# Performance work log

Measured on AMD Instinct MI355X. Metric: run time of the kernel, lower is better.

## Reference

```python
import jax, jax.numpy as jnp
import numpy as np

B, NUM_OBJ, R, D, C = 1024, 128, 32, 512, 7  # scans, obj slots, rel samples, feat dim, rel classes
N = NUM_OBJ + R  # 160 graph nodes per scan


def setup_inputs() -> dict:
    key = jax.random.key(0)
    ks = jax.random.split(key, 8)
    obj_feats = jax.random.normal(ks[0], (B, NUM_OBJ, D), jnp.float32)
    pairs = jax.random.randint(ks[1], (B, R, 2), 0, NUM_OBJ, dtype=jnp.int32)
    init = lambda k, shape, fan_in: jax.random.normal(k, shape, jnp.float32) / np.float32(np.sqrt(fan_in))
    return {
        "obj_feats": obj_feats,
        "pairs": pairs,
        "fuse_w": init(ks[2], (2 * D, D), 2 * D), "fuse_b": jnp.zeros((D,), jnp.float32),
        "gcn_w": init(ks[3], (D, D), D), "gcn_b": jnp.zeros((D,), jnp.float32),
        "fc1_w": init(ks[4], (D, 256), D), "fc1_b": jnp.zeros((256,), jnp.float32),
        "fc2_w": init(ks[5], (256, 128), 256), "fc2_b": jnp.zeros((128,), jnp.float32),
        "fc3_w": init(ks[6], (128, C), 128), "fc3_b": jnp.zeros((C,), jnp.float32),
    }


def reference(obj_feats, pairs, fuse_w, fuse_b, gcn_w, gcn_b,
              fc1_w, fc1_b, fc2_w, fc2_b, fc3_w, fc3_b):
    # --- init_rel_node (pos_fuse=False): fuse sub/obj features per sampled pair ---
    sub = jnp.take_along_axis(obj_feats, pairs[:, :, 0:1], axis=1)  # [B,R,D]
    obj = jnp.take_along_axis(obj_feats, pairs[:, :, 1:2], axis=1)  # [B,R,D]
    init_rel = jnp.concatenate([sub, obj], axis=-1) @ fuse_w + fuse_b  # [B,R,D]

    # --- X: object node feats in rows [0,NUM_OBJ), rel node feats in rows [NUM_OBJ,N) ---
    X = jnp.concatenate([obj_feats, init_rel], axis=1)  # [B,N,D]

    # --- A: get_graph_gcn_with_rel -- scatter 4 directed edges per pair ---
    b_idx = jnp.arange(B)[:, None]                      # [B,1]
    ridx = NUM_OBJ + jnp.arange(R)[None, :]             # [1,R] rel node index j+num_obj
    p0, p1 = pairs[:, :, 0], pairs[:, :, 1]             # [B,R]
    A = jnp.zeros((B, N, N), jnp.float32)
    A = A.at[b_idx, p0, ridx].set(1.0)
    A = A.at[b_idx, ridx, p1].set(1.0)
    A = A.at[b_idx, p1, ridx].set(1.0)
    A = A.at[b_idx, ridx, p0].set(1.0)

    # --- simpleGCN: relu((A @ X) W + b) ---
    H = jax.nn.relu(jnp.einsum('bnm,bmd->bnd', A, X) @ gcn_w + gcn_b)  # [B,N,D]

    # --- residual: GCN rel-node output + init rel feats ---
    rel_feat = H[:, NUM_OBJ:, :] + init_rel  # [B,R,D]

    # --- proxi_detector (dropout = identity, eval behavior) ---
    h = jax.nn.relu(rel_feat @ fc1_w + fc1_b)
    h = jax.nn.relu(h @ fc2_w + fc2_b)
    logits = h @ fc3_w + fc3_b  # [B,R,C]
    return jax.nn.softmax(logits, axis=-1)
```

## Files before the change

### kernel.cpp

```cpp
#include <hip/hip_runtime.h>
#include <hip/hip_bf16.h>

#define B_    1024
#define NOBJ  128
#define RREL  32
#define DIM   512
#define MTOT  32768

typedef __bf16 bf16x8 __attribute__((ext_vector_type(8)));
typedef float  f32x4  __attribute__((ext_vector_type(4)));

__device__ __forceinline__ unsigned short f2bf(float f) {
    unsigned int u = __float_as_uint(f);
    u += 0x7FFFu + ((u >> 16) & 1u);
    return (unsigned short)(u >> 16);
}
__device__ __forceinline__ float bf2f(unsigned short h) {
    return __uint_as_float(((unsigned int)h) << 16);
}

__device__ __forceinline__ void load16_to_lds(const unsigned short* g, unsigned short* l) {
    __builtin_amdgcn_global_load_lds((const __attribute__((address_space(1))) void*)g,
                                     (__attribute__((address_space(3))) void*)l,
                                     16, 0, 0);
}

__global__ __launch_bounds__(256) void gather_kernel(
        const float* __restrict__ obj, const int* __restrict__ pairs,
        unsigned short* __restrict__ As, unsigned short* __restrict__ Msum) {
    int t = threadIdx.x;
    int base = blockIdx.x * 8;
    for (int rr = 0; rr < 8; ++rr) {
        int m  = base + rr;
        int b  = m >> 5;
        int p0 = pairs[(m << 1) + 0];
        int p1 = pairs[(m << 1) + 1];
        const float* srow = obj + (size_t)(b * NOBJ + p0) * DIM;
        const float* orow = obj + (size_t)(b * NOBJ + p1) * DIM;
        float2 s2 = *(const float2*)(srow + 2 * t);
        float2 o2 = *(const float2*)(orow + 2 * t);
        size_t arow = (size_t)m * 1024;
        *(ushort2*)(As + arow + 2 * t)       = make_ushort2(f2bf(s2.x), f2bf(s2.y));
        *(ushort2*)(As + arow + DIM + 2 * t) = make_ushort2(f2bf(o2.x), f2bf(o2.y));
        float mx = s2.x, my = s2.y;
        if (p0 != p1) { mx += o2.x; my += o2.y; }
        *(ushort2*)(Msum + (size_t)m * DIM + 2 * t) = make_ushort2(f2bf(mx), f2bf(my));
    }
}

__global__ __launch_bounds__(256) void transpose_tile(
        const float* __restrict__ in, unsigned short* __restrict__ out,
        int K, int N) {
    __shared__ float t32[32][33];
    int t  = threadIdx.x;
    int tx = t & 31, ty = t >> 5;
    int bk = blockIdx.x * 32, bn = blockIdx.y * 32;
#pragma unroll
    for (int i = 0; i < 4; ++i)
        t32[ty + i * 8][tx] = in[(size_t)(bk + ty + i * 8) * N + bn + tx];
    __syncthreads();
#pragma unroll
    for (int i = 0; i < 4; ++i)
        out[(size_t)(bn + ty + i * 8) * K + bk + tx] = f2bf(t32[tx][ty + i * 8]);
}

__global__ __launch_bounds__(256) void gemm_fused12(
        const unsigned short* __restrict__ As,
        const unsigned short* __restrict__ Msum,
        const unsigned short* __restrict__ WfT,
        const unsigned short* __restrict__ WgT,
        const float* __restrict__ fuse_b, const float* __restrict__ gcn_b,
        unsigned short* __restrict__ rf) {
    __shared__ __align__(16) unsigned short ldsA[128 * 32];
    __shared__ __align__(16) unsigned short ldsB[128 * 32];

    int tid  = threadIdx.x;
    int wid  = tid >> 6;
    int lane = tid & 63;
    int wm   = wid & 1;
    int wn   = wid >> 1;
    int m0   = blockIdx.x * 128;
    int n0   = blockIdx.y * 128;

    f32x4 accF[4][4], accG[4][4];
#pragma unroll
    for (int i = 0; i < 4; ++i)
#pragma unroll
        for (int j = 0; j < 4; ++j)
#pragma unroll
            for (int k = 0; k < 4; ++k) { accF[i][j][k] = 0.0f; accG[i][j][k] = 0.0f; }

    int r = tid >> 2, c = tid & 3;
    unsigned short* la0 = ldsA + wid * 512;
    unsigned short* la1 = ldsA + 2048 + wid * 512;
    unsigned short* lb0 = ldsB + wid * 512;
    unsigned short* lb1 = ldsB + 2048 + wid * 512;

    int arow = wm * 64 + (lane & 15);
    int brow = wn * 64 + (lane & 15);
    int koff = (lane >> 4) * 8;

    {
        const unsigned short* ag0 = As + (size_t)(m0 + r)      * 1024 + c * 8;
        const unsigned short* ag1 = As + (size_t)(m0 + 64 + r) * 1024 + c * 8;
        const unsigned short* bg0 = WfT + (size_t)(n0 + r)      * 1024 + c * 8;
        const unsigned short* bg1 = WfT + (size_t)(n0 + 64 + r) * 1024 + c * 8;
        for (int k0 = 0; k0 < 1024; k0 += 32) {
            __syncthreads();
            load16_to_lds(ag0 + k0, la0);
            load16_to_lds(ag1 + k0, la1);
            load16_to_lds(bg0 + k0, lb0);
            load16_to_lds(bg1 + k0, lb1);
            __syncthreads();
            bf16x8 a[4], b[4];
#pragma unroll
            for (int i = 0; i < 4; ++i)
                a[i] = *(const bf16x8*)(ldsA + (arow + i * 16) * 32 + koff);
#pragma unroll
            for (int j = 0; j < 4; ++j)
                b[j] = *(const bf16x8*)(ldsB + (brow + j * 16) * 32 + koff);
#pragma unroll
            for (int i = 0; i < 4; ++i)
#pragma unroll
                for (int j = 0; j < 4; ++j)
                    accF[i][j] = __builtin_amdgcn_mfma_f32_16x16x32_bf16(a[i], b[j], accF[i][j], 0, 0, 0);
        }
    }
    {
        const unsigned short* ag0 = Msum + (size_t)(m0 + r)      * 512 + c * 8;
        const unsigned short* ag1 = Msum + (size_t)(m0 + 64 + r) * 512 + c * 8;
        const unsigned short* bg0 = WgT + (size_t)(n0 + r)      * 512 + c * 8;
        const unsigned short* bg1 = WgT + (size_t)(n0 + 64 + r) * 512 + c * 8;
        for (int k0 = 0; k0 < 512; k0 += 32) {
            __syncthreads();
            load16_to_lds(ag0 + k0, la0);
            load16_to_lds(ag1 + k0, la1);
            load16_to_lds(bg0 + k0, lb0);
            load16_to_lds(bg1 + k0, lb1);
            __syncthreads();
            bf16x8 a[4], b[4];
#pragma unroll
            for (int i = 0; i < 4; ++i)
                a[i] = *(const bf16x8*)(ldsA + (arow + i * 16) * 32 + koff);
#pragma unroll
            for (int j = 0; j < 4; ++j)
                b[j] = *(const bf16x8*)(ldsB + (brow + j * 16) * 32 + koff);
#pragma unroll
            for (int i = 0; i < 4; ++i)
#pragma unroll
                for (int j = 0; j < 4; ++j)
                    accG[i][j] = __builtin_amdgcn_mfma_f32_16x16x32_bf16(a[i], b[j], accG[i][j], 0, 0, 0);
        }
    }

    int crow  = wm * 64 + (lane >> 4) * 4;
    int ccol0 = wn * 64 + (lane & 15);
    float bf_[4], bg_[4];
#pragma unroll
    for (int j = 0; j < 4; ++j) {
        bf_[j] = fuse_b[n0 + ccol0 + j * 16];
        bg_[j] = gcn_b [n0 + ccol0 + j * 16];
    }
#pragma unroll
    for (int i = 0; i < 4; ++i)
#pragma unroll
        for (int j = 0; j < 4; ++j) {
            int col = n0 + ccol0 + j * 16;
#pragma unroll
            for (int jj = 0; jj < 4; ++jj) {
                int row = m0 + crow + i * 16 + jj;
                float v = fmaxf(accG[i][j][jj] + bg_[j], 0.0f) + accF[i][j][jj] + bf_[j];
                rf[(size_t)row * 512 + col] = f2bf(v);
            }
        }
}

#define H1S 136
__global__ __launch_bounds__(256) void tail_kernel(
        const unsigned short* __restrict__ rf,
        const unsigned short* __restrict__ W1T,
        const unsigned short* __restrict__ W2T,
        const float* __restrict__ b1, const float* __restrict__ b2,
        const float* __restrict__ w3, const float* __restrict__ b3,
        float* __restrict__ out) {
    __shared__ __align__(16) unsigned short ldsA[128 * 32];
    __shared__ __align__(16) unsigned short ldsB[128 * 32];
    __shared__ __align__(16) unsigned short ldsH1[128 * H1S];
    __shared__ __align__(16) unsigned short ldsH2[128 * H1S];
    __shared__ float ldsW3[128 * 7];
    __shared__ float ldsB3[7];

    int tid  = threadIdx.x;
    int wid  = tid >> 6;
    int lane = tid & 63;
    int wm   = wid & 1;
    int wn   = wid >> 1;
    int m0   = blockIdx.x * 128;

    for (int i = tid; i < 128 * 7; i += 256) ldsW3[i] = w3[i];
    if (tid < 7) ldsB3[tid] = b3[tid];

    int r = tid >> 2, c = tid & 3;
    unsigned short* la0 = ldsA + wid * 512;
    unsigned short* la1 = ldsA + 2048 + wid * 512;
    unsigned short* lb0 = ldsB + wid * 512;
    unsigned short* lb1 = ldsB + 2048 + wid * 512;

    int arow = wm * 64 + (lane & 15);
    int brow = wn * 64 + (lane & 15);
    int koff = (lane >> 4) * 8;
    int crow  = wm * 64 + (lane >> 4) * 4;
    int ccol0 = wn * 64 + (lane & 15);

    const unsigned short* ag0 = rf + (size_t)(m0 + r)      * 512 + c * 8;
    const unsigned short* ag1 = rf + (size_t)(m0 + 64 + r) * 512 + c * 8;

    f32x4 acc2[4][4];
#pragma unroll
    for (int i = 0; i < 4; ++i)
#pragma unroll
        for (int j = 0; j < 4; ++j)
#pragma unroll
            for (int k = 0; k < 4; ++k) acc2[i][j][k] = 0.0f;

    for (int nt = 0; nt < 2; ++nt) {
        int n0 = nt * 128;
        f32x4 acc1[4][4];
#pragma unroll
        for (int i = 0; i < 4; ++i)
#pragma unroll
            for (int j = 0; j < 4; ++j)
#pragma unroll
                for (int k = 0; k < 4; ++k) acc1[i][j][k] = 0.0f;

        const unsigned short* bg0 = W1T + (size_t)(n0 + r)      * 512 + c * 8;
        const unsigned short* bg1 = W1T + (size_t)(n0 + 64 + r) * 512 + c * 8;
        for (int k0 = 0; k0 < 512; k0 += 32) {
            __syncthreads();
            load16_to_lds(ag0 + k0, la0);
            load16_to_lds(ag1 + k0, la1);
            load16_to_lds(bg0 + k0, lb0);
            load16_to_lds(bg1 + k0, lb1);
            __syncthreads();
            bf16x8 a[4], b[4];
#pragma unroll
            for (int i = 0; i < 4; ++i)
                a[i] = *(const bf16x8*)(ldsA + (arow + i * 16) * 32 + koff);
#pragma unroll
            for (int j = 0; j < 4; ++j)
                b[j] = *(const bf16x8*)(ldsB + (brow + j * 16) * 32 + koff);
#pragma unroll
            for (int i = 0; i < 4; ++i)
#pragma unroll
                for (int j = 0; j < 4; ++j)
                    acc1[i][j] = __builtin_amdgcn_mfma_f32_16x16x32_bf16(a[i], b[j], acc1[i][j], 0, 0, 0);
        }
        __syncthreads();
#pragma unroll
        for (int i = 0; i < 4; ++i)
#pragma unroll
            for (int j = 0; j < 4; ++j) {
                int col = ccol0 + j * 16;
                float bb = b1[n0 + col];
#pragma unroll
                for (int jj = 0; jj < 4; ++jj) {
                    int row = crow + i * 16 + jj;
                    float v = fmaxf(acc1[i][j][jj] + bb, 0.0f);
                    ldsH1[row * H1S + col] = f2bf(v);
                }
            }
        __syncthreads();
        const unsigned short* wg0 = W2T + (size_t)r        * 256 + n0 + c * 8;
        const unsigned short* wg1 = W2T + (size_t)(64 + r) * 256 + n0 + c * 8;
        for (int k0 = 0; k0 < 128; k0 += 32) {
            __syncthreads();
            load16_to_lds(wg0 + k0, lb0);
            load16_to_lds(wg1 + k0, lb1);
            __syncthreads();
            bf16x8 a[4], b[4];
#pragma unroll
            for (int i = 0; i < 4; ++i)
                a[i] = *(const bf16x8*)(ldsH1 + (arow + i * 16) * H1S + k0 + koff);
#pragma unroll
            for (int j = 0; j < 4; ++j)
                b[j] = *(const bf16x8*)(ldsB + (brow + j * 16) * 32 + koff);
#pragma unroll
            for (int i = 0; i < 4; ++i)
#pragma unroll
                for (int j = 0; j < 4; ++j)
                    acc2[i][j] = __builtin_amdgcn_mfma_f32_16x16x32_bf16(a[i], b[j], acc2[i][j], 0, 0, 0);
        }
        __syncthreads();
    }

#pragma unroll
    for (int i = 0; i < 4; ++i)
#pragma unroll
        for (int j = 0; j < 4; ++j) {
            int col = ccol0 + j * 16;
            float bb = b2[col];
#pragma unroll
            for (int jj = 0; jj < 4; ++jj) {
                int row = crow + i * 16 + jj;
                float v = fmaxf(acc2[i][j][jj] + bb, 0.0f);
                ldsH2[row * H1S + col] = f2bf(v);
            }
        }
    __syncthreads();

    if (tid < 128) {
        const unsigned short* hrow = ldsH2 + tid * H1S;
        float accv[7];
#pragma unroll
        for (int cc = 0; cc < 7; ++cc) accv[cc] = ldsB3[cc];
        for (int k = 0; k < 128; ++k) {
            float f = bf2f(hrow[k]);
#pragma unroll
            for (int cc = 0; cc < 7; ++cc)
                accv[cc] = fmaf(f, ldsW3[k * 7 + cc], accv[cc]);
        }
        float mx = accv[0];
#pragma unroll
        for (int cc = 1; cc < 7; ++cc) mx = fmaxf(mx, accv[cc]);
        float sum = 0.f;
#pragma unroll
        for (int cc = 0; cc < 7; ++cc) { accv[cc] = __expf(accv[cc] - mx); sum += accv[cc]; }
        float inv = 1.0f / sum;
#pragma unroll
        for (int cc = 0; cc < 7; ++cc) out[(size_t)(m0 + tid) * 7 + cc] = accv[cc] * inv;
    }
}

extern "C" void kernel_launch(void* const* d_in, const int* in_sizes, int n_in,
                              void* d_out, int out_size, void* d_ws, size_t ws_size,
                              hipStream_t stream) {
    (void)in_sizes; (void)n_in; (void)out_size; (void)ws_size;
    const float* obj    = (const float*)d_in[0];
    const int*   pairs  = (const int*)  d_in[1];
    const float* fuse_w = (const float*)d_in[2];
    const float* fuse_b = (const float*)d_in[3];
    const float* gcn_w  = (const float*)d_in[4];
    const float* gcn_b  = (const float*)d_in[5];
    const float* fc1_w  = (const float*)d_in[6];
    const float* fc1_b  = (const float*)d_in[7];
    const float* fc2_w  = (const float*)d_in[8];
    const float* fc2_b  = (const float*)d_in[9];
    const float* fc3_w  = (const float*)d_in[10];
    const float* fc3_b  = (const float*)d_in[11];
    float* out = (float*)d_out;

    char* ws = (char*)d_ws;
    unsigned short* As   = (unsigned short*)(ws);
    unsigned short* Msum = (unsigned short*)(ws + (64u  << 20));
    unsigned short* rf   = (unsigned short*)(ws + (96u  << 20));
    unsigned short* WfT  = (unsigned short*)(ws + (128u << 20));
    unsigned short* WgT  = (unsigned short*)(ws + (129u << 20));
    unsigned short* W1T  = (unsigned short*)(ws + (130u << 20));
    unsigned short* W2T  = (unsigned short*)(ws + (131u << 20));

    gather_kernel<<<MTOT / 8, 256, 0, stream>>>(obj, pairs, As, Msum);
    transpose_tile<<<dim3(1024 / 32, 512 / 32), 256, 0, stream>>>(fuse_w, WfT, 1024, 512);
    transpose_tile<<<dim3(512  / 32, 512 / 32), 256, 0, stream>>>(gcn_w,  WgT, 512,  512);
    transpose_tile<<<dim3(512  / 32, 256 / 32), 256, 0, stream>>>(fc1_w,  W1T, 512,  256);
    transpose_tile<<<dim3(256  / 32, 128 / 32), 256, 0, stream>>>(fc2_w,  W2T, 256,  128);

    gemm_fused12<<<dim3(MTOT / 128, 4), 256, 0, stream>>>(
        As, Msum, WfT, WgT, fuse_b, gcn_b, rf);

    tail_kernel<<<MTOT / 128, 256, 0, stream>>>(
        rf, W1T, W2T, fc1_b, fc2_b, fc3_w, fc3_b, out);
}
```

Baseline: 470.2 us.

## Restructure MLP tail kernel, merge weight transposes, widen gather loads

The tail kernel now handles 64 rows per block instead of 128. It computes all 256 fc1 columns in a single pass and splits fc2 over K across warp pairs, with a reduction through LDS. The fc3 stage and softmax are spread over all 256 threads with shuffle reductions, and LDS is reused through a shared pool. Separately, the four weight transpose launches are merged into one kernel, the gather uses float4 loads, and launch_bounds occupancy hints are added to the GEMM kernels. Together these aim to raise parallelism in the tail and cut launch overhead, at the cost of an extra LDS reduction and a larger shared memory footprint.

```diff
diff --git a/kernel.cpp b/kernel.cpp
--- a/kernel.cpp
+++ b/kernel.cpp
@@ -9,17 +9,18 @@
 
 typedef __bf16 bf16x8 __attribute__((ext_vector_type(8)));
 typedef float  f32x4  __attribute__((ext_vector_type(4)));
-
-__device__ __forceinline__ unsigned short f2bf(float f) {
+typedef unsigned short us;
+
+__device__ __forceinline__ us f2bf(float f) {
     unsigned int u = __float_as_uint(f);
     u += 0x7FFFu + ((u >> 16) & 1u);
-    return (unsigned short)(u >> 16);
-}
-__device__ __forceinline__ float bf2f(unsigned short h) {
+    return (us)(u >> 16);
+}
+__device__ __forceinline__ float bf2f(us h) {
     return __uint_as_float(((unsigned int)h) << 16);
 }
 
-__device__ __forceinline__ void load16_to_lds(const unsigned short* g, unsigned short* l) {
+__device__ __forceinline__ void load16_to_lds(const us* g, us* l) {
     __builtin_amdgcn_global_load_lds((const __attribute__((address_space(1))) void*)g,
                                      (__attribute__((address_space(3))) void*)l,
                                      16, 0, 0);
@@ -27,34 +28,50 @@
 
 __global__ __launch_bounds__(256) void gather_kernel(
         const float* __restrict__ obj, const int* __restrict__ pairs,
-        unsigned short* __restrict__ As, unsigned short* __restrict__ Msum) {
+        us* __restrict__ As, us* __restrict__ Msum) {
     int t = threadIdx.x;
+    int g = t >> 7;
+    int c = t & 127;
     int base = blockIdx.x * 8;
-    for (int rr = 0; rr < 8; ++rr) {
-        int m  = base + rr;
+#pragma unroll
+    for (int rr = 0; rr < 4; ++rr) {
+        int m  = base + rr * 2 + g;
         int b  = m >> 5;
         int p0 = pairs[(m << 1) + 0];
         int p1 = pairs[(m << 1) + 1];
-        const float* srow = obj + (size_t)(b * NOBJ + p0) * DIM;
-        const float* orow = obj + (size_t)(b * NOBJ + p1) * DIM;
-        float2 s2 = *(const float2*)(srow + 2 * t);
-        float2 o2 = *(const float2*)(orow + 2 * t);
+        const float4* srow = (const float4*)(obj + (size_t)(b * NOBJ + p0) * DIM);
+        const float4* orow = (const float4*)(obj + (size_t)(b * NOBJ + p1) * DIM);
+        float4 s4 = srow[c];
+        float4 o4 = orow[c];
         size_t arow = (size_t)m * 1024;
-        *(ushort2*)(As + arow + 2 * t)       = make_ushort2(f2bf(s2.x), f2bf(s2.y));
-        *(ushort2*)(As + arow + DIM + 2 * t) = make_ushort2(f2bf(o2.x), f2bf(o2.y));
-        float mx = s2.x, my = s2.y;
-        if (p0 != p1) { mx += o2.x; my += o2.y; }
-        *(ushort2*)(Msum + (size_t)m * DIM + 2 * t) = make_ushort2(f2bf(mx), f2bf(my));
-    }
-}
-
-__global__ __launch_bounds__(256) void transpose_tile(
-        const float* __restrict__ in, unsigned short* __restrict__ out,
-        int K, int N) {
+        ushort4 sb = make_ushort4(f2bf(s4.x), f2bf(s4.y), f2bf(s4.z), f2bf(s4.w));
+        ushort4 ob = make_ushort4(f2bf(o4.x), f2bf(o4.y), f2bf(o4.z), f2bf(o4.w));
+        *(ushort4*)(As + arow + c * 4)       = sb;
+        *(ushort4*)(As + arow + 512 + c * 4) = ob;
+        float4 mz = s4;
+        if (p0 != p1) { mz.x += o4.x; mz.y += o4.y; mz.z += o4.z; mz.w += o4.w; }
+        *(ushort4*)(Msum + (size_t)m * 512 + c * 4) =
+            make_ushort4(f2bf(mz.x), f2bf(mz.y), f2bf(mz.z), f2bf(mz.w));
+    }
+}
+
+__global__ __launch_bounds__(256) void prep_weights(
+        const float* __restrict__ fw, const float* __restrict__ gw,
+        const float* __restrict__ w1, const float* __restrict__ w2,
+        us* __restrict__ WfT, us* __restrict__ WgT,
+        us* __restrict__ W1T, us* __restrict__ W2T) {
     __shared__ float t32[32][33];
+    int id = blockIdx.x;
+    const float* in; us* out; int K, N, local;
+    if (id < 512)      { in = fw; out = WfT; K = 1024; N = 512; local = id; }
+    else if (id < 768) { in = gw; out = WgT; K = 512;  N = 512; local = id - 512; }
+    else if (id < 896) { in = w1; out = W1T; K = 512;  N = 256; local = id - 768; }
+    else               { in = w2; out = W2T; K = 256;  N = 128; local = id - 896; }
+    int tilesN = N >> 5;
+    int bk = (local / tilesN) * 32;
+    int bn = (local % tilesN) * 32;
     int t  = threadIdx.x;
     int tx = t & 31, ty = t >> 5;
-    int bk = blockIdx.x * 32, bn = blockIdx.y * 32;
 #pragma unroll
     for (int i = 0; i < 4; ++i)
         t32[ty + i * 8][tx] = in[(size_t)(bk + ty + i * 8) * N + bn + tx];
@@ -64,15 +81,15 @@
         out[(size_t)(bn + ty + i * 8) * K + bk + tx] = f2bf(t32[tx][ty + i * 8]);
 }
 
-__global__ __launch_bounds__(256) void gemm_fused12(
-        const unsigned short* __restrict__ As,
-        const unsigned short* __restrict__ Msum,
-        const unsigned short* __restrict__ WfT,
-        const unsigned short* __restrict__ WgT,
+__global__ __launch_bounds__(256, 2) void gemm_fused12(
+        const us* __restrict__ As,
+        const us* __restrict__ Msum,
+        const us* __restrict__ WfT,
+        const us* __restrict__ WgT,
         const float* __restrict__ fuse_b, const float* __restrict__ gcn_b,
-        unsigned short* __restrict__ rf) {
-    __shared__ __align__(16) unsigned short ldsA[128 * 32];
-    __shared__ __align__(16) unsigned short ldsB[128 * 32];
+        us* __restrict__ rf) {
+    __shared__ __align__(16) us ldsA[128 * 32];
+    __shared__ __align__(16) us ldsB[128 * 32];
 
     int tid  = threadIdx.x;
     int wid  = tid >> 6;
@@ -91,20 +108,20 @@
             for (int k = 0; k < 4; ++k) { accF[i][j][k] = 0.0f; accG[i][j][k] = 0.0f; }
 
     int r = tid >> 2, c = tid & 3;
-    unsigned short* la0 = ldsA + wid * 512;
-    unsigned short* la1 = ldsA + 2048 + wid * 512;
-    unsigned short* lb0 = ldsB + wid * 512;
-    unsigned short* lb1 = ldsB + 2048 + wid * 512;
+    us* la0 = ldsA + wid * 512;
+    us* la1 = ldsA + 2048 + wid * 512;
+    us* lb0 = ldsB + wid * 512;
+    us* lb1 = ldsB + 2048 + wid * 512;
 
     int arow = wm * 64 + (lane & 15);
     int brow = wn * 64 + (lane & 15);
     int koff = (lane >> 4) * 8;
 
     {
-        const unsigned short* ag0 = As + (size_t)(m0 + r)      * 1024 + c * 8;
-        const unsigned short* ag1 = As + (size_t)(m0 + 64 + r) * 1024 + c * 8;
-        const unsigned short* bg0 = WfT + (size_t)(n0 + r)      * 1024 + c * 8;
-        const unsigned short* bg1 = WfT + (size_t)(n0 + 64 + r) * 1024 + c * 8;
+        const us* ag0 = As + (size_t)(m0 + r)      * 1024 + c * 8;
+        const us* ag1 = As + (size_t)(m0 + 64 + r) * 1024 + c * 8;
+        const us* bg0 = WfT + (size_t)(n0 + r)      * 1024 + c * 8;
+        const us* bg1 = WfT + (size_t)(n0 + 64 + r) * 1024 + c * 8;
         for (int k0 = 0; k0 < 1024; k0 += 32) {
             __syncthreads();
             load16_to_lds(ag0 + k0, la0);
@@ -127,10 +144,10 @@
         }
     }
     {
-        const unsigned short* ag0 = Msum + (size_t)(m0 + r)      * 512 + c * 8;
-        const unsigned short* ag1 = Msum + (size_t)(m0 + 64 + r) * 512 + c * 8;
-        const unsigned short* bg0 = WgT + (size_t)(n0 + r)      * 512 + c * 8;
-        const unsigned short* bg1 = WgT + (size_t)(n0 + 64 + r) * 512 + c * 8;
+        const us* ag0 = Msum + (size_t)(m0 + r)      * 512 + c * 8;
+        const us* ag1 = Msum + (size_t)(m0 + 64 + r) * 512 + c * 8;
+        const us* bg0 = WgT + (size_t)(n0 + r)      * 512 + c * 8;
+        const us* bg1 = WgT + (size_t)(n0 + 64 + r) * 512 + c * 8;
         for (int k0 = 0; k0 < 512; k0 += 32) {
             __syncthreads();
             load16_to_lds(ag0 + k0, la0);
@@ -175,159 +192,179 @@
         }
 }
 
-#define H1S 136
-__global__ __launch_bounds__(256) void tail_kernel(
-        const unsigned short* __restrict__ rf,
-        const unsigned short* __restrict__ W1T,
-        const unsigned short* __restrict__ W2T,
+#define H1S 264
+#define H2S 136
+__global__ __launch_bounds__(256, 2) void tail_kernel(
+        const us* __restrict__ rf,
+        const us* __restrict__ W1T,
+        const us* __restrict__ W2T,
         const float* __restrict__ b1, const float* __restrict__ b2,
         const float* __restrict__ w3, const float* __restrict__ b3,
         float* __restrict__ out) {
-    __shared__ __align__(16) unsigned short ldsA[128 * 32];
-    __shared__ __align__(16) unsigned short ldsB[128 * 32];
-    __shared__ __align__(16) unsigned short ldsH1[128 * H1S];
-    __shared__ __align__(16) unsigned short ldsH2[128 * H1S];
-    __shared__ float ldsW3[128 * 7];
-    __shared__ float ldsB3[7];
+    __shared__ __align__(16) unsigned char pool[57888];
+    us*    sA   = (us*)(pool);
+    us*    sB   = (us*)(pool + 4096);
+    us*    sH2  = (us*)(pool);
+    us*    sH1  = (us*)(pool + 20480);
+    float* sRed = (float*)(pool + 20480);
+    float* sW3  = (float*)(pool + 54272);
+    float* sB3  = (float*)(pool + 57856);
 
     int tid  = threadIdx.x;
     int wid  = tid >> 6;
     int lane = tid & 63;
-    int wm   = wid & 1;
-    int wn   = wid >> 1;
-    int m0   = blockIdx.x * 128;
-
-    for (int i = tid; i < 128 * 7; i += 256) ldsW3[i] = w3[i];
-    if (tid < 7) ldsB3[tid] = b3[tid];
+    int m0   = blockIdx.x * 64;
+
+    for (int i = tid; i < 128 * 7; i += 256) sW3[i] = w3[i];
+    if (tid < 7) sB3[tid] = b3[tid];
 
     int r = tid >> 2, c = tid & 3;
-    unsigned short* la0 = ldsA + wid * 512;
-    unsigned short* la1 = ldsA + 2048 + wid * 512;
-    unsigned short* lb0 = ldsB + wid * 512;
-    unsigned short* lb1 = ldsB + 2048 + wid * 512;
-
-    int arow = wm * 64 + (lane & 15);
-    int brow = wn * 64 + (lane & 15);
     int koff = (lane >> 4) * 8;
-    int crow  = wm * 64 + (lane >> 4) * 4;
-    int ccol0 = wn * 64 + (lane & 15);
-
-    const unsigned short* ag0 = rf + (size_t)(m0 + r)      * 512 + c * 8;
-    const unsigned short* ag1 = rf + (size_t)(m0 + 64 + r) * 512 + c * 8;
-
-    f32x4 acc2[4][4];
+    int l15  = lane & 15;
+
+    f32x4 acc1[4][4];
 #pragma unroll
     for (int i = 0; i < 4; ++i)
 #pragma unroll
         for (int j = 0; j < 4; ++j)
 #pragma unroll
-            for (int k = 0; k < 4; ++k) acc2[i][j][k] = 0.0f;
-
-    for (int nt = 0; nt < 2; ++nt) {
-        int n0 = nt * 128;
-        f32x4 acc1[4][4];
-#pragma unroll
-        for (int i = 0; i < 4; ++i)
+            for (int k = 0; k < 4; ++k) acc1[i][j][k] = 0.0f;
+
+    {
+        const us* ag = rf + (size_t)(m0 + r) * 512 + c * 8;
+        us* la = sA + wid * 512;
+        for (int k0 = 0; k0 < 512; k0 += 32) {
+            __syncthreads();
+            load16_to_lds(ag + k0, la);
+#pragma unroll
+            for (int q = 0; q < 4; ++q)
+                load16_to_lds(W1T + (size_t)(q * 64 + r) * 512 + k0 + c * 8,
+                              sB + q * 2048 + wid * 512);
+            __syncthreads();
+            bf16x8 a[4], b[4];
+#pragma unroll
+            for (int i = 0; i < 4; ++i)
+                a[i] = *(const bf16x8*)(sA + (l15 + i * 16) * 32 + koff);
 #pragma unroll
             for (int j = 0; j < 4; ++j)
-#pragma unroll
-                for (int k = 0; k < 4; ++k) acc1[i][j][k] = 0.0f;
-
-        const unsigned short* bg0 = W1T + (size_t)(n0 + r)      * 512 + c * 8;
-        const unsigned short* bg1 = W1T + (size_t)(n0 + 64 + r) * 512 + c * 8;
-        for (int k0 = 0; k0 < 512; k0 += 32) {
-            __syncthreads();
-            load16_to_lds(ag0 + k0, la0);
-            load16_to_lds(ag1 + k0, la1);
-            load16_to_lds(bg0 + k0, lb0);
-            load16_to_lds(bg1 + k0, lb1);
-            __syncthreads();
-            bf16x8 a[4], b[4];
-#pragma unroll
-            for (int i = 0; i < 4; ++i)
-                a[i] = *(const bf16x8*)(ldsA + (arow + i * 16) * 32 + koff);
-#pragma unroll
-            for (int j = 0; j < 4; ++j)
-                b[j] = *(const bf16x8*)(ldsB + (brow + j * 16) * 32 + koff);
+                b[j] = *(const bf16x8*)(sB + (wid * 64 + j * 16 + l15) * 32 + koff);
 #pragma unroll
             for (int i = 0; i < 4; ++i)
 #pragma unroll
                 for (int j = 0; j < 4; ++j)
                     acc1[i][j] = __builtin_amdgcn_mfma_f32_16x16x32_bf16(a[i], b[j], acc1[i][j], 0, 0, 0);
         }
+    }
+#pragma unroll
+    for (int i = 0; i < 4; ++i)
+#pragma unroll
+        for (int j = 0; j < 4; ++j) {
+            int col = wid * 64 + j * 16 + l15;
+            float bb = b1[col];
+#pragma unroll
+            for (int jj = 0; jj < 4; ++jj) {
+                int row = i * 16 + (lane >> 4) * 4 + jj;
+                sH1[row * H1S + col] = f2bf(fmaxf(acc1[i][j][jj] + bb, 0.0f));
+            }
+        }
+
+    int nw = wid & 1, kw = wid >> 1;
+    f32x4 acc2[4][4];
+#pragma unroll
+    for (int i = 0; i < 4; ++i)
+#pragma unroll
+        for (int j = 0; j < 4; ++j)
+#pragma unroll
+            for (int k = 0; k < 4; ++k) acc2[i][j][k] = 0.0f;
+
+    for (int t = 0; t < 4; ++t) {
         __syncthreads();
 #pragma unroll
+        for (int s = 0; s < 2; ++s)
+#pragma unroll
+            for (int q = 0; q < 2; ++q)
+                load16_to_lds(W2T + (size_t)(q * 64 + r) * 256 + s * 128 + t * 32 + c * 8,
+                              sB + s * 4096 + q * 2048 + wid * 512);
+        __syncthreads();
+        bf16x8 a[4], b[4];
+#pragma unroll
         for (int i = 0; i < 4; ++i)
+            a[i] = *(const bf16x8*)(sH1 + (l15 + i * 16) * H1S + kw * 128 + t * 32 + koff);
+#pragma unroll
+        for (int j = 0; j < 4; ++j)
+            b[j] = *(const bf16x8*)(sB + kw * 4096 + (nw * 64 + j * 16 + l15) * 32 + koff);
+#pragma unroll
+        for (int i = 0; i < 4; ++i)
+#pragma unroll
+            for (int j = 0; j < 4; ++j)
+                acc2[i][j] = __builtin_amdgcn_mfma_f32_16x16x32_bf16(a[i], b[j], acc2[i][j], 0, 0, 0);
+    }
+    __syncthreads();
+    if (kw == 1) {
+#pragma unroll
+        for (int i = 0; i < 4; ++i)
 #pragma unroll
             for (int j = 0; j < 4; ++j) {
-                int col = ccol0 + j * 16;
-                float bb = b1[n0 + col];
+                int col = nw * 64 + j * 16 + l15;
 #pragma unroll
                 for (int jj = 0; jj < 4; ++jj) {
-                    int row = crow + i * 16 + jj;
-                    float v = fmaxf(acc1[i][j][jj] + bb, 0.0f);
-                    ldsH1[row * H1S + col] = f2bf(v);
+                    int row = i * 16 + (lane >> 4) * 4 + jj;
+                    sRed[row * 132 + col] = acc2[i][j][jj];
                 }
             }
-        __syncthreads();
-        const unsigned short* wg0 = W2T + (size_t)r        * 256 + n0 + c * 8;
-        const unsigned short* wg1 = W2T + (size_t)(64 + r) * 256 + n0 + c * 8;
-        for (int k0 = 0; k0 < 128; k0 += 32) {
-            __syncthreads();
-            load16_to_lds(wg0 + k0, lb0);
-            load16_to_lds(wg1 + k0, lb1);
-            __syncthreads();
-            bf16x8 a[4], b[4];
-#pragma unroll
-            for (int i = 0; i < 4; ++i)
-                a[i] = *(const bf16x8*)(ldsH1 + (arow + i * 16) * H1S + k0 + koff);
-#pragma unroll
-            for (int j = 0; j < 4; ++j)
-                b[j] = *(const bf16x8*)(ldsB + (brow + j * 16) * 32 + koff);
-#pragma unroll
-            for (int i = 0; i < 4; ++i)
-#pragma unroll
-                for (int j = 0; j < 4; ++j)
-                    acc2[i][j] = __builtin_amdgcn_mfma_f32_16x16x32_bf16(a[i], b[j], acc2[i][j], 0, 0, 0);
-        }
-        __syncthreads();
-    }
-
-#pragma unroll
-    for (int i = 0; i < 4; ++i)
-#pragma unroll
-        for (int j = 0; j < 4; ++j) {
-            int col = ccol0 + j * 16;
-            float bb = b2[col];
-#pragma unroll
-            for (int jj = 0; jj < 4; ++jj) {
-                int row = crow + i * 16 + jj;
-                float v = fmaxf(acc2[i][j][jj] + bb, 0.0f);
-                ldsH2[row * H1S + col] = f2bf(v);
+    }
+    __syncthreads();
+    if (kw == 0) {
+#pragma unroll
+        for (int i = 0; i < 4; ++i)
+#pragma unroll
+            for (int j = 0; j < 4; ++j) {
+                int col = nw * 64 + j * 16 + l15;
+                float bb = b2[col];
+#pragma unroll
+                for (int jj = 0; jj < 4; ++jj) {
+                    int row = i * 16 + (lane >> 4) * 4 + jj;
+                    float v = acc2[i][j][jj] + sRed[row * 132 + col] + bb;
+                    sH2[row * H2S + col] = f2bf(fmaxf(v, 0.0f));
+                }
             }
-        }
+    }
     __syncthreads();
 
-    if (tid < 128) {
-        const unsigned short* hrow = ldsH2 + tid * H1S;
-        float accv[7];
-#pragma unroll
-        for (int cc = 0; cc < 7; ++cc) accv[cc] = ldsB3[cc];
-        for (int k = 0; k < 128; ++k) {
-            float f = bf2f(hrow[k]);
-#pragma unroll
-            for (int cc = 0; cc < 7; ++cc)
-                accv[cc] = fmaf(f, ldsW3[k * 7 + cc], accv[cc]);
-        }
-        float mx = accv[0];
-#pragma unroll
-        for (int cc = 1; cc < 7; ++cc) mx = fmaxf(mx, accv[cc]);
+    int row = tid >> 2;
+    int p   = tid & 3;
+    float accv[7];
+#pragma unroll
+    for (int cc = 0; cc < 7; ++cc) accv[cc] = 0.0f;
+    const us* hrow = sH2 + row * H2S + p * 32;
+    for (int kk = 0; kk < 8; ++kk) {
+        ushort4 u = *(const ushort4*)(hrow + kk * 4);
+        float f0 = bf2f(u.x), f1 = bf2f(u.y), f2 = bf2f(u.z), f3 = bf2f(u.w);
+        int k = p * 32 + kk * 4;
+#pragma unroll
+        for (int cc = 0; cc < 7; ++cc) {
+            accv[cc] = fmaf(f0, sW3[(k + 0) * 7 + cc], accv[cc]);
+            accv[cc] = fmaf(f1, sW3[(k + 1) * 7 + cc], accv[cc]);
+            accv[cc] = fmaf(f2, sW3[(k + 2) * 7 + cc], accv[cc]);
+            accv[cc] = fmaf(f3, sW3[(k + 3) * 7 + cc], accv[cc]);
+        }
+    }
+#pragma unroll
+    for (int cc = 0; cc < 7; ++cc) {
+        accv[cc] += __shfl_xor(accv[cc], 1);
+        accv[cc] += __shfl_xor(accv[cc], 2);
+    }
+    if (p == 0) {
+        float mx = accv[0] + sB3[0];
+        float lg[7];
+#pragma unroll
+        for (int cc = 0; cc < 7; ++cc) { lg[cc] = accv[cc] + sB3[cc]; mx = fmaxf(mx, lg[cc]); }
         float sum = 0.f;
 #pragma unroll
-        for (int cc = 0; cc < 7; ++cc) { accv[cc] = __expf(accv[cc] - mx); sum += accv[cc]; }
+        for (int cc = 0; cc < 7; ++cc) { lg[cc] = __expf(lg[cc] - mx); sum += lg[cc]; }
         float inv = 1.0f / sum;
 #pragma unroll
-        for (int cc = 0; cc < 7; ++cc) out[(size_t)(m0 + tid) * 7 + cc] = accv[cc] * inv;
+        for (int cc = 0; cc < 7; ++cc) out[(size_t)(m0 + row) * 7 + cc] = lg[cc] * inv;
     }
 }
 
@@ -350,23 +387,21 @@
     float* out = (float*)d_out;
 
     char* ws = (char*)d_ws;
-    unsigned short* As   = (unsigned short*)(ws);
-    unsigned short* Msum = (unsigned short*)(ws + (64u  << 20));
-    unsigned short* rf   = (unsigned short*)(ws + (96u  << 20));
-    unsigned short* WfT  = (unsigned short*)(ws + (128u << 20));
-    unsigned short* WgT  = (unsigned short*)(ws + (129u << 20));
-    unsigned short* W1T  = (unsigned short*)(ws + (130u << 20));
-    unsigned short* W2T  = (unsigned short*)(ws + (131u << 20));
+    us* As   = (us*)(ws);
+    us* Msum = (us*)(ws + (64u  << 20));
+    us* rf   = (us*)(ws + (96u  << 20));
+    us* WfT  = (us*)(ws + (128u << 20));
+    us* WgT  = (us*)(ws + (129u << 20));
+    us* W1T  = (us*)(ws + (130u << 20));
+    us* W2T  = (us*)(ws + (131u << 20));
 
     gather_kernel<<<MTOT / 8, 256, 0, stream>>>(obj, pairs, As, Msum);
-    transpose_tile<<<dim3(1024 / 32, 512 / 32), 256, 0, stream>>>(fuse_w, WfT, 1024, 512);
-    transpose_tile<<<dim3(512  / 32, 512 / 32), 256, 0, stream>>>(gcn_w,  WgT, 512,  512);
-    transpose_tile<<<dim3(512  / 32, 256 / 32), 256, 0, stream>>>(fc1_w,  W1T, 512,  256);
-    transpose_tile<<<dim3(256  / 32, 128 / 32), 256, 0, stream>>>(fc2_w,  W2T, 256,  128);
+    prep_weights<<<928, 256, 0, stream>>>(fuse_w, gcn_w, fc1_w, fc2_w,
+                                          WfT, WgT, W1T, W2T);
 
     gemm_fused12<<<dim3(MTOT / 128, 4), 256, 0, stream>>>(
         As, Msum, WfT, WgT, fuse_b, gcn_b, rf);
 
-    tail_kernel<<<MTOT / 128, 256, 0, stream>>>(
+    tail_kernel<<<MTOT / 64, 256, 0, stream>>>(
         rf, W1T, W2T, fc1_b, fc2_b, fc3_w, fc3_b, out);
 }
```

Result: faster. 447.7 us (-4.8%).
